# Optimization experiments

Measured on AMD Instinct MI355X. Metric: run time of the kernel, lower is better.

## Reference

```python
import jax, jax.numpy as jnp
import numpy as np

N_NODES = 100000
N_EDGES = 1600000
D = 64
N_LAYERS = 3
N_GRAPHS = 128
BN_EPS = 1e-5


def setup_inputs() -> dict:
    key = jax.random.key(0)
    k_x, k_e, k_b, k_w = jax.random.split(key, 4)
    x = jax.random.normal(k_x, (N_NODES, D), dtype=jnp.float32)
    edge_index = jax.random.randint(k_e, (2, N_EDGES), 0, N_NODES, dtype=jnp.int64)
    batch = jnp.sort(jax.random.randint(k_b, (N_NODES,), 0, N_GRAPHS, dtype=jnp.int64))
    Ws = jax.random.normal(k_w, (N_LAYERS, D, D), dtype=jnp.float32) * (1.0 / np.sqrt(D))
    bs = jnp.zeros((N_LAYERS, D), dtype=jnp.float32)
    gammas = jnp.ones((N_LAYERS, D), dtype=jnp.float32)
    betas = jnp.zeros((N_LAYERS, D), dtype=jnp.float32)
    return {"x": x, "edge_index": edge_index, "batch": batch,
            "Ws": Ws, "bs": bs, "gammas": gammas, "betas": betas}


def reference(x, edge_index, batch, Ws, bs, gammas, betas):
    N = x.shape[0]
    # GCN: add self-loops, symmetric normalization deg^{-1/2}_src * deg^{-1/2}_dst
    loop = jnp.arange(N, dtype=edge_index.dtype)
    src = jnp.concatenate([edge_index[0], loop])  # [E+N]
    dst = jnp.concatenate([edge_index[1], loop])
    deg = jax.ops.segment_sum(jnp.ones_like(dst, dtype=x.dtype), dst, num_segments=N)
    dinv = jnp.where(deg > 0, jax.lax.rsqrt(deg), 0.0)
    norm = dinv[src] * dinv[dst]  # [E+N]

    h = x
    for l in range(N_LAYERS):
        t = h @ Ws[l]                                    # [N,D] dense transform
        msg = t[src] * norm[:, None]                     # gather + scale [E+N,D]
        t = jax.ops.segment_sum(msg, dst, num_segments=N) + bs[l]
        # BatchNorm1d (training-style batch statistics, biased variance)
        mean = jnp.mean(t, axis=0)
        var = jnp.mean((t - mean) ** 2, axis=0)
        t = (t - mean) * jax.lax.rsqrt(var + BN_EPS) * gammas[l] + betas[l]
        h = jax.nn.relu(t)

    # global mean pool over graphs
    sums = jax.ops.segment_sum(h, batch, num_segments=N_GRAPHS)        # [G,D]
    counts = jax.ops.segment_sum(jnp.ones((N,), dtype=h.dtype), batch, num_segments=N_GRAPHS)
    return sums / jnp.maximum(counts, 1.0)[:, None]
```

## Files before the change

### kernel.cpp

```cpp
#include <hip/hip_runtime.h>
#include <hip/hip_bf16.h>

typedef __hip_bfloat16 bf16;
typedef short bf16x8 __attribute__((ext_vector_type(8)));
typedef float f32x4 __attribute__((ext_vector_type(4)));

#define NN 100000
#define NE 1600000
#define DD 64
#define NL 3
#define NG 128
#define BN_EPS 1e-5f
#define SCAN_BLK 98
#define TILE_ROWS 64
#define LSW 72
#define NT ((NN + TILE_ROWS - 1) / TILE_ROWS)
#define GB_NODES 48
#define GB_BLOCKS ((NN + GB_NODES - 1) / GB_NODES)
#define ECAP 1664
#define CSW_CAP (NE + 7 * NN)

#define NBUK 391
#define BUK_CAP 4608
#define OVF_CAP 8192
#define EPB 4096
#define NBB ((NE + EPB - 1) / EPB)

__device__ __forceinline__ int ld_src(const int* ei, int e, int is32) {
    return is32 ? ei[e] : ei[2 * e];
}
__device__ __forceinline__ int ld_dst(const int* ei, int e, int is32) {
    return is32 ? ei[NE + e] : ei[2 * NE + 2 * e];
}
__device__ __forceinline__ int ld_batch(const int* b, int n, int is32) {
    return is32 ? b[n] : b[2 * n];
}
__device__ __forceinline__ float bf2f(unsigned short u) {
    return __uint_as_float(((unsigned int)u) << 16);
}
__device__ __forceinline__ unsigned short f2bf(float x) {
    bf16 b = __float2bfloat16(x);
    return *reinterpret_cast<unsigned short*>(&b);
}
__device__ __forceinline__ void split_bf16(float x, unsigned short& hi, unsigned short& lo) {
    hi = f2bf(x);
    lo = f2bf(x - bf2f(hi));
}
__device__ __forceinline__ int pad8(int d) { return (d + 7) & ~7; }

__global__ __launch_bounds__(256) void bin_kernel(const int* __restrict__ ei,
                                                  int* __restrict__ deg_cnt,
                                                  int* __restrict__ bukcnt,
                                                  int* __restrict__ staging,
                                                  int* __restrict__ ovf_cnt,
                                                  int2* __restrict__ ovf) {
    __shared__ int hist[NBUK];
    __shared__ int base[NBUK];
    __shared__ int s_e;
    if (threadIdx.x == 0) s_e = 0;
    for (int i = threadIdx.x; i < NBUK; i += 256) hist[i] = 0;
    __syncthreads();
    if (ei[2 * threadIdx.x + 1] != 0) atomicOr(&s_e, 1);
    __syncthreads();
    int is32 = s_e;

    int e0 = blockIdx.x * EPB;
    int myb[16], mypack[16], myidx[16];
#pragma unroll
    for (int k = 0; k < 16; ++k) {
        int e = e0 + k * 256 + threadIdx.x;
        myb[k] = -1;
        if (e < NE) {
            int s = ld_src(ei, e, is32), d = ld_dst(ei, e, is32);
            int b = d >> 8;
            myb[k] = b;
            mypack[k] = (s << 8) | (d & 255);
            myidx[k] = atomicAdd(&hist[b], 1);
        }
    }
    __syncthreads();
    for (int i = threadIdx.x; i < NBUK; i += 256)
        if (hist[i]) base[i] = atomicAdd(&bukcnt[i], hist[i]);
    __syncthreads();
#pragma unroll
    for (int k = 0; k < 16; ++k) {
        if (myb[k] >= 0) {
            int slot = base[myb[k]] + myidx[k];
            if (slot < BUK_CAP) {
                staging[myb[k] * BUK_CAP + slot] = mypack[k];
            } else {
                int d = (myb[k] << 8) | (mypack[k] & 255);
                atomicAdd(&deg_cnt[d], 1);
                int o = atomicAdd(ovf_cnt, 1);
                if (o < OVF_CAP) ovf[o] = make_int2(mypack[k] >> 8, d);
            }
        }
    }
}

__global__ __launch_bounds__(256) void scan_part_kernel(int* __restrict__ deg_cnt,
                                                        const int* __restrict__ bukcnt,
                                                        const int* __restrict__ staging,
                                                        int* __restrict__ blocksum,
                                                        float* __restrict__ dinv) {
    __shared__ int hist[1024];
    __shared__ int s[256];
    for (int i = threadIdx.x; i < 1024; i += 256) hist[i] = 0;
    __syncthreads();
    int b4 = blockIdx.x * 4;
#pragma unroll
    for (int j = 0; j < 4; ++j) {
        int bk = b4 + j;
        if (bk < NBUK) {
            int n = min(bukcnt[bk], BUK_CAP);
            const int* st = staging + bk * BUK_CAP;
            for (int i = threadIdx.x; i < n; i += 256)
                atomicAdd(&hist[(j << 8) | (st[i] & 255)], 1);
        }
    }
    __syncthreads();
    int base = blockIdx.x * 1024 + threadIdx.x * 4;
    int t = 0;
    if (base < NN) {
        int4 ov = *(const int4*)(deg_cnt + base);
        int4 hv = *(const int4*)(hist + threadIdx.x * 4);
        int4 v = make_int4(ov.x + hv.x, ov.y + hv.y, ov.z + hv.z, ov.w + hv.w);
        *(int4*)(deg_cnt + base) = v;
        t = pad8(v.x) + pad8(v.y) + pad8(v.z) + pad8(v.w);
        float4 dv = make_float4(rsqrtf((float)v.x + 1.f), rsqrtf((float)v.y + 1.f),
                                rsqrtf((float)v.z + 1.f), rsqrtf((float)v.w + 1.f));
        *(float4*)(dinv + base) = dv;
    }
    s[threadIdx.x] = t;
    __syncthreads();
    for (int off = 128; off > 0; off >>= 1) {
        if (threadIdx.x < off) s[threadIdx.x] += s[threadIdx.x + off];
        __syncthreads();
    }
    if (threadIdx.x == 0) blocksum[blockIdx.x] = s[0];
}

__global__ __launch_bounds__(256) void scan_write_kernel(int* __restrict__ deg_cnt,
                                                         const int* __restrict__ blocksum,
                                                         int* __restrict__ rowptr) {
    __shared__ int sb[128];
    __shared__ int s[256];
    if (threadIdx.x < 128)
        sb[threadIdx.x] = (threadIdx.x < SCAN_BLK) ? blocksum[threadIdx.x] : 0;
    __syncthreads();
    for (int off = 1; off < 128; off <<= 1) {
        int a = 0;
        if (threadIdx.x < 128 && threadIdx.x >= off) a = sb[threadIdx.x - off];
        __syncthreads();
        if (threadIdx.x < 128) sb[threadIdx.x] += a;
        __syncthreads();
    }
    int blockpre = (blockIdx.x == 0) ? 0 : sb[blockIdx.x - 1];
    if (blockIdx.x == SCAN_BLK - 1 && threadIdx.x == 0)
        rowptr[NN] = sb[SCAN_BLK - 1];

    int base = blockIdx.x * 1024 + threadIdx.x * 4;
    int4 v = make_int4(0, 0, 0, 0);
    if (base < NN) v = *(const int4*)(deg_cnt + base);
    int p0 = pad8(v.x), p1 = pad8(v.y), p2 = pad8(v.z), p3 = pad8(v.w);
    int t = p0 + p1 + p2 + p3;
    s[threadIdx.x] = t;
    for (int off = 1; off < 256; off <<= 1) {
        __syncthreads();
        int a = (threadIdx.x >= off) ? s[threadIdx.x - off] : 0;
        __syncthreads();
        s[threadIdx.x] += a;
    }
    __syncthreads();
    int pre = blockpre + s[threadIdx.x] - t;
    if (base < NN) {
        rowptr[base] = pre;
        rowptr[base + 1] = pre + p0;
        rowptr[base + 2] = pre + p0 + p1;
        rowptr[base + 3] = pre + p0 + p1 + p2;
        *(int4*)(deg_cnt + base) = make_int4(0, 0, 0, 0);
    }
}

__global__ __launch_bounds__(256) void scatter_kernel(const int* __restrict__ bukcnt,
                                                      const int* __restrict__ staging,
                                                      const int* __restrict__ ovf_cnt,
                                                      const int2* __restrict__ ovf,
                                                      const int* __restrict__ rowptr,
                                                      int* __restrict__ cursor,
                                                      int* __restrict__ csw) {
    int b = blockIdx.x;
    if (b == NBUK) {
        int n = min(*ovf_cnt, OVF_CAP);
        for (int i = threadIdx.x; i < n; i += 256) {
            int2 e = ovf[i];
            int pos = rowptr[e.y] + atomicAdd(&cursor[e.y], 1);
            csw[pos] = (e.x + 1) << 7;
        }
        return;
    }
    int n = min(bukcnt[b], BUK_CAP);
    int nb = b << 8;
    const int* st = staging + b * BUK_CAP;
    for (int i = threadIdx.x; i < n; i += 256) {
        int v = st[i];
        int d = nb + (v & 255);
        int pos = rowptr[d] + atomicAdd(&cursor[d], 1);
        csw[pos] = ((v >> 8) + 1) << 7;
    }
}

__global__ __launch_bounds__(256) void gemm_kernel(const float* __restrict__ h,
                                                   const float* __restrict__ W,
                                                   const float* __restrict__ dinv,
                                                   const float* __restrict__ accum_prev,
                                                   const float* __restrict__ gamma,
                                                   const float* __restrict__ beta,
                                                   int use_bn, float alpha,
                                                   bf16* __restrict__ t,
                                                   float* __restrict__ accum_l) {
    if (blockIdx.x == 0 && threadIdx.x < 128) accum_l[threadIdx.x] = 0.f;

    __shared__ unsigned short ls_hi[TILE_ROWS * LSW];
    __shared__ unsigned short ls_lo[TILE_ROWS * LSW];
    __shared__ float ssc[DD], ssh[DD], sdinv[TILE_ROWS];
    int tid = threadIdx.x;
    if (tid < 64) {
        if (use_bn) {
            float S = accum_prev[tid], Q = accum_prev[64 + tid];
            float mean = S / (float)NN;
            float var = fmaxf(Q / (float)NN - mean * mean, 0.f);
            float sc = gamma[tid] * rsqrtf(var + BN_EPS);
            ssc[tid] = sc;
            ssh[tid] = beta[tid] - mean * sc;
        } else {
            ssc[tid] = 1.f;
            ssh[tid] = 0.f;
        }
    }

    int lane = tid & 63;
    int wv = tid >> 6;
    int lr = lane & 15;
    int lg = lane >> 4;

    bf16x8 bhi[2][4], blo[2][4];
#pragma unroll
    for (int ks = 0; ks < 2; ++ks)
#pragma unroll
        for (int nt = 0; nt < 4; ++nt)
#pragma unroll
            for (int e = 0; e < 8; ++e) {
                float wval = W[(ks * 32 + lg * 8 + e) * DD + nt * 16 + lr];
                unsigned short hi, lo;
                split_bf16(wval, hi, lo);
                bhi[ks][nt][e] = (short)hi;
                blo[ks][nt][e] = (short)lo;
            }
    __syncthreads();

    for (int tile = blockIdx.x; tile < NT; tile += gridDim.x) {
        int row0 = tile * TILE_ROWS;
        int nrows = min(TILE_ROWS, NN - row0);
        if (tid < 64) sdinv[tid] = (row0 + tid < NN) ? dinv[row0 + tid] : 0.f;
#pragma unroll
        for (int it = 0; it < 4; ++it) {
            int flat = (tid + it * 256) * 4;
            int gflat = row0 * DD + flat;
            if (gflat < NN * DD) {
                float4 hv = *(const float4*)(h + gflat);
                int c0 = flat & 63;
                float4 s4 = *(const float4*)(ssc + c0);
                float4 b4 = *(const float4*)(ssh + c0);
                float x0 = hv.x * s4.x + b4.x;
                float x1 = hv.y * s4.y + b4.y;
                float x2 = hv.z * s4.z + b4.z;
                float x3 = hv.w * s4.w + b4.w;
                x0 = fmaxf(x0, x0 * alpha);
                x1 = fmaxf(x1, x1 * alpha);
                x2 = fmaxf(x2, x2 * alpha);
                x3 = fmaxf(x3, x3 * alpha);
                unsigned short h0, l0, h1, l1, h2, l2, h3, l3;
                split_bf16(x0, h0, l0);
                split_bf16(x1, h1, l1);
                split_bf16(x2, h2, l2);
                split_bf16(x3, h3, l3);
                int row = flat >> 6;
                *(ushort4*)(ls_hi + row * LSW + c0) = make_ushort4(h0, h1, h2, h3);
                *(ushort4*)(ls_lo + row * LSW + c0) = make_ushort4(l0, l1, l2, l3);
            }
        }
        __syncthreads();

        f32x4 acc[4];
#pragma unroll
        for (int nt = 0; nt < 4; ++nt) acc[nt] = (f32x4){0.f, 0.f, 0.f, 0.f};

#pragma unroll
        for (int ks = 0; ks < 2; ++ks) {
            int aoff = (wv * 16 + lr) * LSW + ks * 32 + lg * 8;
            bf16x8 a_hi = *(const bf16x8*)(ls_hi + aoff);
            bf16x8 a_lo = *(const bf16x8*)(ls_lo + aoff);
#pragma unroll
            for (int nt = 0; nt < 4; ++nt) {
                acc[nt] = __builtin_amdgcn_mfma_f32_16x16x32_bf16(a_hi, bhi[ks][nt],
                                                                  acc[nt], 0, 0, 0);
                acc[nt] = __builtin_amdgcn_mfma_f32_16x16x32_bf16(a_hi, blo[ks][nt],
                                                                  acc[nt], 0, 0, 0);
                acc[nt] = __builtin_amdgcn_mfma_f32_16x16x32_bf16(a_lo, bhi[ks][nt],
                                                                  acc[nt], 0, 0, 0);
            }
        }
        __syncthreads();

#pragma unroll
        for (int nt = 0; nt < 4; ++nt)
#pragma unroll
            for (int rg = 0; rg < 4; ++rg) {
                int orow = wv * 16 + lg * 4 + rg;
                ls_hi[orow * LSW + nt * 16 + lr] = f2bf(acc[nt][rg] * sdinv[orow]);
            }
        __syncthreads();
#pragma unroll
        for (int it = 0; it < 2; ++it) {
            int flat8 = (tid + it * 256) * 8;
            int row = flat8 >> 6, c = flat8 & 63;
            if (row < nrows) {
                uint4 v = *(const uint4*)(ls_hi + row * LSW + c);
                *(uint4*)((unsigned short*)t + (size_t)(row0 + row) * DD + c) = v;
            }
        }
        __syncthreads();
    }
}

__device__ __forceinline__ void batch8(const int* __restrict__ ep, int j,
                                       const char* __restrict__ tbase, int f2,
                                       float& acc) {
    int4 a0 = *(const int4*)(ep + j);
    int4 a1 = *(const int4*)(ep + j + 4);
    unsigned short r[8];
    r[0] = *(const unsigned short*)(tbase + (unsigned)(a0.x + f2));
    r[1] = *(const unsigned short*)(tbase + (unsigned)(a0.y + f2));
    r[2] = *(const unsigned short*)(tbase + (unsigned)(a0.z + f2));
    r[3] = *(const unsigned short*)(tbase + (unsigned)(a0.w + f2));
    r[4] = *(const unsigned short*)(tbase + (unsigned)(a1.x + f2));
    r[5] = *(const unsigned short*)(tbase + (unsigned)(a1.y + f2));
    r[6] = *(const unsigned short*)(tbase + (unsigned)(a1.z + f2));
    r[7] = *(const unsigned short*)(tbase + (unsigned)(a1.w + f2));
    float s01 = bf2f(r[0]) + bf2f(r[1]), s23 = bf2f(r[2]) + bf2f(r[3]);
    float s45 = bf2f(r[4]) + bf2f(r[5]), s67 = bf2f(r[6]) + bf2f(r[7]);
    acc += (s01 + s23) + (s45 + s67);
}

__device__ __forceinline__ void batch8x2(const int* __restrict__ ep, int jA, int jB,
                                         const char* __restrict__ tbase, int f2,
                                         float& accA, float& accB) {
    int4 aA0 = *(const int4*)(ep + jA), aA1 = *(const int4*)(ep + jA + 4);
    int4 aB0 = *(const int4*)(ep + jB), aB1 = *(const int4*)(ep + jB + 4);
    unsigned short rA[8], rB[8];
    rA[0] = *(const unsigned short*)(tbase + (unsigned)(aA0.x + f2));
    rA[1] = *(const unsigned short*)(tbase + (unsigned)(aA0.y + f2));
    rA[2] = *(const unsigned short*)(tbase + (unsigned)(aA0.z + f2));
    rA[3] = *(const unsigned short*)(tbase + (unsigned)(aA0.w + f2));
    rA[4] = *(const unsigned short*)(tbase + (unsigned)(aA1.x + f2));
    rA[5] = *(const unsigned short*)(tbase + (unsigned)(aA1.y + f2));
    rA[6] = *(const unsigned short*)(tbase + (unsigned)(aA1.z + f2));
    rA[7] = *(const unsigned short*)(tbase + (unsigned)(aA1.w + f2));
    rB[0] = *(const unsigned short*)(tbase + (unsigned)(aB0.x + f2));
    rB[1] = *(const unsigned short*)(tbase + (unsigned)(aB0.y + f2));
    rB[2] = *(const unsigned short*)(tbase + (unsigned)(aB0.z + f2));
    rB[3] = *(const unsigned short*)(tbase + (unsigned)(aB0.w + f2));
    rB[4] = *(const unsigned short*)(tbase + (unsigned)(aB1.x + f2));
    rB[5] = *(const unsigned short*)(tbase + (unsigned)(aB1.y + f2));
    rB[6] = *(const unsigned short*)(tbase + (unsigned)(aB1.z + f2));
    rB[7] = *(const unsigned short*)(tbase + (unsigned)(aB1.w + f2));
    float sA01 = bf2f(rA[0]) + bf2f(rA[1]), sA23 = bf2f(rA[2]) + bf2f(rA[3]);
    float sA45 = bf2f(rA[4]) + bf2f(rA[5]), sA67 = bf2f(rA[6]) + bf2f(rA[7]);
    accA += (sA01 + sA23) + (sA45 + sA67);
    float sB01 = bf2f(rB[0]) + bf2f(rB[1]), sB23 = bf2f(rB[2]) + bf2f(rB[3]);
    float sB45 = bf2f(rB[4]) + bf2f(rB[5]), sB67 = bf2f(rB[6]) + bf2f(rB[7]);
    accB += (sB01 + sB23) + (sB45 + sB67);
}

__device__ __forceinline__ void batch8x4(const int* __restrict__ ep, int jA, int jB,
                                         int jC, int jD,
                                         const char* __restrict__ tbase, int f2,
                                         float& accA, float& accB, float& accC,
                                         float& accD) {
    int4 aA0 = *(const int4*)(ep + jA), aA1 = *(const int4*)(ep + jA + 4);
    int4 aB0 = *(const int4*)(ep + jB), aB1 = *(const int4*)(ep + jB + 4);
    int4 aC0 = *(const int4*)(ep + jC), aC1 = *(const int4*)(ep + jC + 4);
    int4 aD0 = *(const int4*)(ep + jD), aD1 = *(const int4*)(ep + jD + 4);
    unsigned short rA[8], rB[8], rC[8], rD[8];
    rA[0] = *(const unsigned short*)(tbase + (unsigned)(aA0.x + f2));
    rA[1] = *(const unsigned short*)(tbase + (unsigned)(aA0.y + f2));
    rA[2] = *(const unsigned short*)(tbase + (unsigned)(aA0.z + f2));
    rA[3] = *(const unsigned short*)(tbase + (unsigned)(aA0.w + f2));
    rA[4] = *(const unsigned short*)(tbase + (unsigned)(aA1.x + f2));
    rA[5] = *(const unsigned short*)(tbase + (unsigned)(aA1.y + f2));
    rA[6] = *(const unsigned short*)(tbase + (unsigned)(aA1.z + f2));
    rA[7] = *(const unsigned short*)(tbase + (unsigned)(aA1.w + f2));
    rB[0] = *(const unsigned short*)(tbase + (unsigned)(aB0.x + f2));
    rB[1] = *(const unsigned short*)(tbase + (unsigned)(aB0.y + f2));
    rB[2] = *(const unsigned short*)(tbase + (unsigned)(aB0.z + f2));
    rB[3] = *(const unsigned short*)(tbase + (unsigned)(aB0.w + f2));
    rB[4] = *(const unsigned short*)(tbase + (unsigned)(aB1.x + f2));
    rB[5] = *(const unsigned short*)(tbase + (unsigned)(aB1.y + f2));
    rB[6] = *(const unsigned short*)(tbase + (unsigned)(aB1.z + f2));
    rB[7] = *(const unsigned short*)(tbase + (unsigned)(aB1.w + f2));
    rC[0] = *(const unsigned short*)(tbase + (unsigned)(aC0.x + f2));
    rC[1] = *(const unsigned short*)(tbase + (unsigned)(aC0.y + f2));
    rC[2] = *(const unsigned short*)(tbase + (unsigned)(aC0.z + f2));
    rC[3] = *(const unsigned short*)(tbase + (unsigned)(aC0.w + f2));
    rC[4] = *(const unsigned short*)(tbase + (unsigned)(aC1.x + f2));
    rC[5] = *(const unsigned short*)(tbase + (unsigned)(aC1.y + f2));
    rC[6] = *(const unsigned short*)(tbase + (unsigned)(aC1.z + f2));
    rC[7] = *(const unsigned short*)(tbase + (unsigned)(aC1.w + f2));
    rD[0] = *(const unsigned short*)(tbase + (unsigned)(aD0.x + f2));
    rD[1] = *(const unsigned short*)(tbase + (unsigned)(aD0.y + f2));
    rD[2] = *(const unsigned short*)(tbase + (unsigned)(aD0.z + f2));
    rD[3] = *(const unsigned short*)(tbase + (unsigned)(aD0.w + f2));
    rD[4] = *(const unsigned short*)(tbase + (unsigned)(aD1.x + f2));
    rD[5] = *(const unsigned short*)(tbase + (unsigned)(aD1.y + f2));
    rD[6] = *(const unsigned short*)(tbase + (unsigned)(aD1.z + f2));
    rD[7] = *(const unsigned short*)(tbase + (unsigned)(aD1.w + f2));
    float sA01 = bf2f(rA[0]) + bf2f(rA[1]), sA23 = bf2f(rA[2]) + bf2f(rA[3]);
    float sA45 = bf2f(rA[4]) + bf2f(rA[5]), sA67 = bf2f(rA[6]) + bf2f(rA[7]);
    accA += (sA01 + sA23) + (sA45 + sA67);
    float sB01 = bf2f(rB[0]) + bf2f(rB[1]), sB23 = bf2f(rB[2]) + bf2f(rB[3]);
    float sB45 = bf2f(rB[4]) + bf2f(rB[5]), sB67 = bf2f(rB[6]) + bf2f(rB[7]);
    accB += (sB01 + sB23) + (sB45 + sB67);
    float sC01 = bf2f(rC[0]) + bf2f(rC[1]), sC23 = bf2f(rC[2]) + bf2f(rC[3]);
    float sC45 = bf2f(rC[4]) + bf2f(rC[5]), sC67 = bf2f(rC[6]) + bf2f(rC[7]);
    accC += (sC01 + sC23) + (sC45 + sC67);
    float sD01 = bf2f(rD[0]) + bf2f(rD[1]), sD23 = bf2f(rD[2]) + bf2f(rD[3]);
    float sD45 = bf2f(rD[4]) + bf2f(rD[5]), sD67 = bf2f(rD[6]) + bf2f(rD[7]);
    accD += (sD01 + sD23) + (sD45 + sD67);
}

__device__ __forceinline__ void run_quad(const int* __restrict__ ep,
                                         const char* __restrict__ tbase, int f2,
                                         int jA, int eA, int jB, int eB,
                                         int jC, int eC, int jD, int eD,
                                         float& accA, float& accB, float& accC,
                                         float& accD) {
    while (jA < eA && jB < eB && jC < eC && jD < eD) {
        batch8x4(ep, jA, jB, jC, jD, tbase, f2, accA, accB, accC, accD);
        jA += 8; jB += 8; jC += 8; jD += 8;
    }
    while (jA < eA && jB < eB) { batch8x2(ep, jA, jB, tbase, f2, accA, accB); jA += 8; jB += 8; }
    while (jC < eC && jD < eD) { batch8x2(ep, jC, jD, tbase, f2, accC, accD); jC += 8; jD += 8; }
    while (jA < eA && jC < eC) { batch8x2(ep, jA, jC, tbase, f2, accA, accC); jA += 8; jC += 8; }
    while (jA < eA && jD < eD) { batch8x2(ep, jA, jD, tbase, f2, accA, accD); jA += 8; jD += 8; }
    while (jB < eB && jC < eC) { batch8x2(ep, jB, jC, tbase, f2, accB, accC); jB += 8; jC += 8; }
    while (jB < eB && jD < eD) { batch8x2(ep, jB, jD, tbase, f2, accB, accD); jB += 8; jD += 8; }
    while (jA < eA) { batch8(ep, jA, tbase, f2, accA); jA += 8; }
    while (jB < eB) { batch8(ep, jB, tbase, f2, accB); jB += 8; }
    while (jC < eC) { batch8(ep, jC, tbase, f2, accC); jC += 8; }
    while (jD < eD) { batch8(ep, jD, tbase, f2, accD); jD += 8; }
}

__global__ __launch_bounds__(256) void gather_kernel(const bf16* __restrict__ t,
                                                     const float* __restrict__ dinv,
                                                     const float* __restrict__ bias,
                                                     const int* __restrict__ rowptr,
                                                     const int* __restrict__ csw,
                                                     float* __restrict__ h,
                                                     float* __restrict__ accum_l) {
    __shared__ __attribute__((aligned(16))) int se[ECAP];
    __shared__ int srp[GB_NODES + 1];
    __shared__ float s_sum[256], s_sq[256];

    int f = threadIdx.x & 63;
    int wv = threadIdx.x >> 6;
    int nb0 = blockIdx.x * GB_NODES;
    int nloc = min(GB_NODES, NN - nb0);

    for (int i = threadIdx.x; i <= nloc; i += 256) srp[i] = rowptr[nb0 + i];
    __syncthreads();
    int ebase = srp[0];
    int nE = srp[nloc] - ebase;
    bool staged = (nE <= ECAP);
    if (staged) {
        for (int i = threadIdx.x * 4; i < nE; i += 1024)
            *(int4*)(se + i) = *(const int4*)(csw + ebase + i);
    }
    __syncthreads();

    const char* tbase = (const char*)t - 128;
    int f2 = f * 2;
    const unsigned short* tf = (const unsigned short*)t + f;
    float bb = bias[f];
    float sum = 0.f, sq = 0.f;

    for (int q = wv; 4 * q < nloc; q += 4) {
        int d0 = 4 * q;
        int nA = nb0 + d0, nB = nA + 1, nC = nA + 2, nD = nA + 3;
        float accA = bf2f(tf[(size_t)nA * DD]);
        float accB = bf2f(tf[(size_t)nB * DD]);
        float accC = bf2f(tf[(size_t)nC * DD]);
        float accD = bf2f(tf[(size_t)nD * DD]);
        int jA = srp[d0] - ebase, eA = srp[d0 + 1] - ebase;
        int jB = eA, eB = srp[d0 + 2] - ebase;
        int jC = eB, eC = srp[d0 + 3] - ebase;
        int jD = eC, eD = srp[d0 + 4] - ebase;

        if (staged)
            run_quad(se, tbase, f2, jA, eA, jB, eB, jC, eC, jD, eD, accA, accB, accC, accD);
        else
            run_quad(csw + ebase, tbase, f2, jA, eA, jB, eB, jC, eC, jD, eD,
                     accA, accB, accC, accD);

        float diA = dinv[nA], diB = dinv[nB], diC = dinv[nC], diD = dinv[nD];
        accA = accA * diA + bb;
        accB = accB * diB + bb;
        accC = accC * diC + bb;
        accD = accD * diD + bb;
        h[(size_t)nA * DD + f] = accA;
        h[(size_t)nB * DD + f] = accB;
        h[(size_t)nC * DD + f] = accC;
        h[(size_t)nD * DD + f] = accD;
        sum += accA + accB + accC + accD;
        sq += accA * accA + accB * accB + accC * accC + accD * accD;
    }
    s_sum[threadIdx.x] = sum;
    s_sq[threadIdx.x] = sq;
    __syncthreads();
    if (threadIdx.x < 64) {
        sum = s_sum[f] + s_sum[64 + f] + s_sum[128 + f] + s_sum[192 + f];
        sq = s_sq[f] + s_sq[64 + f] + s_sq[128 + f] + s_sq[192 + f];
        atomicAdd(&accum_l[f], sum);
        atomicAdd(&accum_l[64 + f], sq);
    }
}

#define POOL_CHUNK 128
__global__ __launch_bounds__(256) void pool_kernel(const float* __restrict__ hraw,
                                                   const float* __restrict__ accum_l,
                                                   const float* __restrict__ gamma,
                                                   const float* __restrict__ beta,
                                                   const int* __restrict__ batch,
                                                   float* __restrict__ pool,
                                                   float* __restrict__ counts) {
    __shared__ float ssc[64], ssh[64];
    __shared__ int s_b;
    if (threadIdx.x == 0) s_b = 0;
    if (threadIdx.x < 64) {
        float S = accum_l[threadIdx.x], Q = accum_l[64 + threadIdx.x];
        float mean = S / (float)NN;
        float var = fmaxf(Q / (float)NN - mean * mean, 0.f);
        float sc = gamma[threadIdx.x] * rsqrtf(var + BN_EPS);
        ssc[threadIdx.x] = sc;
        ssh[threadIdx.x] = beta[threadIdx.x] - mean * sc;
    }
    __syncthreads();
    if (batch[NN - 1024 + 2 * threadIdx.x + 1] != 0) atomicOr(&s_b, 1);
    __syncthreads();
    int is32 = s_b;
    int f = threadIdx.x & 63, rg = threadIdx.x >> 6;
    float sc = ssc[f], sh = ssh[f];
    int base = blockIdx.x * POOL_CHUNK;
    float acc = 0.f, cnt = 0.f;
    int cur = -1;
    for (int i = rg; i < POOL_CHUNK; i += 4) {
        int n = base + i;
        if (n >= NN) break;
        int g = ld_batch(batch, n, is32);
        if (g != cur) {
            if (cur >= 0) {
                atomicAdd(&pool[cur * DD + f], acc);
                if (f == 0) atomicAdd(&counts[cur], cnt);
            }
            acc = 0.f;
            cnt = 0.f;
            cur = g;
        }
        acc += fmaxf(hraw[(size_t)n * DD + f] * sc + sh, 0.f);
        cnt += 1.f;
    }
    if (cur >= 0) {
        atomicAdd(&pool[cur * DD + f], acc);
        if (f == 0) atomicAdd(&counts[cur], cnt);
    }
}

__global__ __launch_bounds__(256) void final_kernel(const float* __restrict__ pool,
                                                    const float* __restrict__ counts,
                                                    float* __restrict__ out) {
    int i = blockIdx.x * 256 + threadIdx.x;
    if (i < NG * DD) {
        int g = i >> 6;
        out[i] = pool[i] / fmaxf(counts[g], 1.0f);
    }
}

extern "C" void kernel_launch(void* const* d_in, const int* in_sizes, int n_in,
                              void* d_out, int out_size, void* d_ws, size_t ws_size,
                              hipStream_t stream) {
    const float* x = (const float*)d_in[0];
    const int* edge_index = (const int*)d_in[1];
    const int* batch = (const int*)d_in[2];
    const float* Ws = (const float*)d_in[3];
    const float* bs = (const float*)d_in[4];
    const float* gammas = (const float*)d_in[5];
    const float* betas = (const float*)d_in[6];
    float* out = (float*)d_out;

    float* h = (float*)d_ws;
    bf16* zrow = (bf16*)(h + (size_t)NN * DD);
    bf16* t = zrow + DD;
    int* csw = (int*)(t + (size_t)NN * DD);
    float* dinv = (float*)(csw + CSW_CAP);
    int* deg_cnt = (int*)(dinv + NN);
    float* pool = (float*)(deg_cnt + NN);
    float* counts = pool + NG * DD;
    int* bukcnt = (int*)(counts + NG);
    int* ovf_cnt = bukcnt + NBUK;
    int* rowptr = ovf_cnt + 1;
    float* accum = (float*)(rowptr + NN + 1);
    int* blocksum = (int*)(accum + NL * 128);
    int2* ovf = (int2*)(blocksum + 128);
    int* staging = (int*)h;

    hipMemsetAsync(deg_cnt, 0, (NN + NG * DD + NG + NBUK + 1) * sizeof(int), stream);
    hipMemsetAsync(csw, 0, (size_t)CSW_CAP * sizeof(int), stream);
    hipMemsetAsync(zrow, 0, DD * sizeof(bf16), stream);

    bin_kernel<<<NBB, 256, 0, stream>>>(edge_index, deg_cnt, bukcnt, staging,
                                        ovf_cnt, ovf);
    scan_part_kernel<<<SCAN_BLK, 256, 0, stream>>>(deg_cnt, bukcnt, staging, blocksum,
                                                   dinv);
    scan_write_kernel<<<SCAN_BLK, 256, 0, stream>>>(deg_cnt, blocksum, rowptr);
    scatter_kernel<<<NBUK + 1, 256, 0, stream>>>(bukcnt, staging, ovf_cnt, ovf, rowptr,
                                                 deg_cnt, csw);

    for (int l = 0; l < NL; ++l) {
        const float* hin = (l == 0) ? x : h;
        float alpha = (l == 0) ? 1.0f : 0.0f;
        gemm_kernel<<<NT, 256, 0, stream>>>(hin, Ws + (size_t)l * DD * DD, dinv,
                                            accum + (l - 1 >= 0 ? l - 1 : 0) * 128,
                                            gammas + (l - 1 >= 0 ? l - 1 : 0) * DD,
                                            betas + (l - 1 >= 0 ? l - 1 : 0) * DD,
                                            (l > 0) ? 1 : 0, alpha, t, accum + l * 128);
        gather_kernel<<<GB_BLOCKS, 256, 0, stream>>>(t, dinv, bs + l * DD, rowptr, csw, h,
                                                     accum + l * 128);
    }

    pool_kernel<<<(NN + POOL_CHUNK - 1) / POOL_CHUNK, 256, 0, stream>>>(
        h, accum + 2 * 128, gammas + 2 * DD, betas + 2 * DD, batch, pool, counts);
    final_kernel<<<(NG * DD + 255) / 256, 256, 0, stream>>>(pool, counts, out);
}
```

Baseline: 494.6 us.

## Fuse scatter with layer-0 GEMM, precompute weight fragments, fold final into pool

```diff
diff --git a/kernel.cpp b/kernel.cpp
--- a/kernel.cpp
+++ b/kernel.cpp
@@ -1,5 +1,6 @@
 #include <hip/hip_runtime.h>
 #include <hip/hip_bf16.h>
+#include <stdint.h>
 
 typedef __hip_bfloat16 bf16;
 typedef short bf16x8 __attribute__((ext_vector_type(8)));
@@ -19,6 +20,7 @@
 #define GB_BLOCKS ((NN + GB_NODES - 1) / GB_NODES)
 #define ECAP 1664
 #define CSW_CAP (NE + 7 * NN)
+#define WFL 8192
 
 #define NBUK 391
 #define BUK_CAP 4608
@@ -142,7 +144,27 @@
 
 __global__ __launch_bounds__(256) void scan_write_kernel(int* __restrict__ deg_cnt,
                                                          const int* __restrict__ blocksum,
-                                                         int* __restrict__ rowptr) {
+                                                         int* __restrict__ rowptr,
+                                                         const float* __restrict__ Ws,
+                                                         unsigned short* __restrict__ wfrag) {
+    if (blockIdx.x >= SCAN_BLK) {
+        int l = blockIdx.x - SCAN_BLK;
+        const float* W = Ws + (size_t)l * DD * DD;
+        unsigned short* wf = wfrag + (size_t)l * WFL;
+        for (int slot = threadIdx.x; slot < 512; slot += 256) {
+            int lane = slot & 63, nt = (slot >> 6) & 3, ks = slot >> 8;
+            int lr = lane & 15, lg = lane >> 4;
+#pragma unroll
+            for (int e = 0; e < 8; ++e) {
+                float wval = W[(ks * 32 + lg * 8 + e) * DD + nt * 16 + lr];
+                unsigned short hi, lo;
+                split_bf16(wval, hi, lo);
+                wf[((0 * 2 + ks) * 4 + nt) * 512 + lane * 8 + e] = hi;
+                wf[((1 * 2 + ks) * 4 + nt) * 512 + lane * 8 + e] = lo;
+            }
+        }
+        return;
+    }
     __shared__ int sb[128];
     __shared__ int s[256];
     if (threadIdx.x < 128)
@@ -182,14 +204,13 @@
     }
 }
 
-__global__ __launch_bounds__(256) void scatter_kernel(const int* __restrict__ bukcnt,
-                                                      const int* __restrict__ staging,
-                                                      const int* __restrict__ ovf_cnt,
-                                                      const int2* __restrict__ ovf,
-                                                      const int* __restrict__ rowptr,
-                                                      int* __restrict__ cursor,
-                                                      int* __restrict__ csw) {
-    int b = blockIdx.x;
+__device__ __forceinline__ void scatter_body(int b, const int* __restrict__ bukcnt,
+                                             const int* __restrict__ staging,
+                                             const int* __restrict__ ovf_cnt,
+                                             const int2* __restrict__ ovf,
+                                             const int* __restrict__ rowptr,
+                                             int* __restrict__ cursor,
+                                             int* __restrict__ csw) {
     if (b == NBUK) {
         int n = min(*ovf_cnt, OVF_CAP);
         for (int i = threadIdx.x; i < n; i += 256) {
@@ -210,20 +231,24 @@
     }
 }
 
-__global__ __launch_bounds__(256) void gemm_kernel(const float* __restrict__ h,
-                                                   const float* __restrict__ W,
-                                                   const float* __restrict__ dinv,
-                                                   const float* __restrict__ accum_prev,
-                                                   const float* __restrict__ gamma,
-                                                   const float* __restrict__ beta,
-                                                   int use_bn, float alpha,
-                                                   bf16* __restrict__ t,
-                                                   float* __restrict__ accum_l) {
-    if (blockIdx.x == 0 && threadIdx.x < 128) accum_l[threadIdx.x] = 0.f;
-
-    __shared__ unsigned short ls_hi[TILE_ROWS * LSW];
-    __shared__ unsigned short ls_lo[TILE_ROWS * LSW];
-    __shared__ float ssc[DD], ssh[DD], sdinv[TILE_ROWS];
+struct GemmSmem {
+    unsigned short ls_hi[TILE_ROWS * LSW];
+    unsigned short ls_lo[TILE_ROWS * LSW];
+    float ssc[DD], ssh[DD], sdinv[TILE_ROWS];
+};
+
+__device__ __forceinline__ void gemm_body(GemmSmem& sm,
+                                          const float* __restrict__ h,
+                                          const unsigned short* __restrict__ wf,
+                                          const float* __restrict__ dinv,
+                                          const float* __restrict__ accum_prev,
+                                          const float* __restrict__ gamma,
+                                          const float* __restrict__ beta,
+                                          int use_bn, float alpha,
+                                          bf16* __restrict__ t,
+                                          float* __restrict__ accum_l,
+                                          int do_zero, int tile0, int tstride) {
+    if (do_zero && threadIdx.x < 128) accum_l[threadIdx.x] = 0.f;
     int tid = threadIdx.x;
     if (tid < 64) {
         if (use_bn) {
@@ -231,11 +256,11 @@
             float mean = S / (float)NN;
             float var = fmaxf(Q / (float)NN - mean * mean, 0.f);
             float sc = gamma[tid] * rsqrtf(var + BN_EPS);
-            ssc[tid] = sc;
-            ssh[tid] = beta[tid] - mean * sc;
+            sm.ssc[tid] = sc;
+            sm.ssh[tid] = beta[tid] - mean * sc;
         } else {
-            ssc[tid] = 1.f;
-            ssh[tid] = 0.f;
+            sm.ssc[tid] = 1.f;
+            sm.ssh[tid] = 0.f;
         }
     }
 
@@ -248,21 +273,16 @@
 #pragma unroll
     for (int ks = 0; ks < 2; ++ks)
 #pragma unroll
-        for (int nt = 0; nt < 4; ++nt)
-#pragma unroll
-            for (int e = 0; e < 8; ++e) {
-                float wval = W[(ks * 32 + lg * 8 + e) * DD + nt * 16 + lr];
-                unsigned short hi, lo;
-                split_bf16(wval, hi, lo);
-                bhi[ks][nt][e] = (short)hi;
-                blo[ks][nt][e] = (short)lo;
-            }
-    __syncthreads();
-
-    for (int tile = blockIdx.x; tile < NT; tile += gridDim.x) {
+        for (int nt = 0; nt < 4; ++nt) {
+            bhi[ks][nt] = *(const bf16x8*)(wf + ((0 * 2 + ks) * 4 + nt) * 512 + lane * 8);
+            blo[ks][nt] = *(const bf16x8*)(wf + ((1 * 2 + ks) * 4 + nt) * 512 + lane * 8);
+        }
+    __syncthreads();
+
+    for (int tile = tile0; tile < NT; tile += tstride) {
         int row0 = tile * TILE_ROWS;
         int nrows = min(TILE_ROWS, NN - row0);
-        if (tid < 64) sdinv[tid] = (row0 + tid < NN) ? dinv[row0 + tid] : 0.f;
+        if (tid < 64) sm.sdinv[tid] = (row0 + tid < NN) ? dinv[row0 + tid] : 0.f;
 #pragma unroll
         for (int it = 0; it < 4; ++it) {
             int flat = (tid + it * 256) * 4;
@@ -270,8 +290,8 @@
             if (gflat < NN * DD) {
                 float4 hv = *(const float4*)(h + gflat);
                 int c0 = flat & 63;
-                float4 s4 = *(const float4*)(ssc + c0);
-                float4 b4 = *(const float4*)(ssh + c0);
+                float4 s4 = *(const float4*)(sm.ssc + c0);
+                float4 b4 = *(const float4*)(sm.ssh + c0);
                 float x0 = hv.x * s4.x + b4.x;
                 float x1 = hv.y * s4.y + b4.y;
                 float x2 = hv.z * s4.z + b4.z;
@@ -286,8 +306,8 @@
                 split_bf16(x2, h2, l2);
                 split_bf16(x3, h3, l3);
                 int row = flat >> 6;
-                *(ushort4*)(ls_hi + row * LSW + c0) = make_ushort4(h0, h1, h2, h3);
-                *(ushort4*)(ls_lo + row * LSW + c0) = make_ushort4(l0, l1, l2, l3);
+                *(ushort4*)(sm.ls_hi + row * LSW + c0) = make_ushort4(h0, h1, h2, h3);
+                *(ushort4*)(sm.ls_lo + row * LSW + c0) = make_ushort4(l0, l1, l2, l3);
             }
         }
         __syncthreads();
@@ -299,8 +319,8 @@
 #pragma unroll
         for (int ks = 0; ks < 2; ++ks) {
             int aoff = (wv * 16 + lr) * LSW + ks * 32 + lg * 8;
-            bf16x8 a_hi = *(const bf16x8*)(ls_hi + aoff);
-            bf16x8 a_lo = *(const bf16x8*)(ls_lo + aoff);
+            bf16x8 a_hi = *(const bf16x8*)(sm.ls_hi + aoff);
+            bf16x8 a_lo = *(const bf16x8*)(sm.ls_lo + aoff);
 #pragma unroll
             for (int nt = 0; nt < 4; ++nt) {
                 acc[nt] = __builtin_amdgcn_mfma_f32_16x16x32_bf16(a_hi, bhi[ks][nt],
@@ -318,7 +338,7 @@
 #pragma unroll
             for (int rg = 0; rg < 4; ++rg) {
                 int orow = wv * 16 + lg * 4 + rg;
-                ls_hi[orow * LSW + nt * 16 + lr] = f2bf(acc[nt][rg] * sdinv[orow]);
+                sm.ls_hi[orow * LSW + nt * 16 + lr] = f2bf(acc[nt][rg] * sm.sdinv[orow]);
             }
         __syncthreads();
 #pragma unroll
@@ -326,12 +346,42 @@
             int flat8 = (tid + it * 256) * 8;
             int row = flat8 >> 6, c = flat8 & 63;
             if (row < nrows) {
-                uint4 v = *(const uint4*)(ls_hi + row * LSW + c);
+                uint4 v = *(const uint4*)(sm.ls_hi + row * LSW + c);
                 *(uint4*)((unsigned short*)t + (size_t)(row0 + row) * DD + c) = v;
             }
         }
         __syncthreads();
     }
+}
+
+__global__ __launch_bounds__(256) void scatter_gemm_kernel(
+    const int* __restrict__ bukcnt, const int* __restrict__ staging,
+    const int* __restrict__ ovf_cnt, const int2* __restrict__ ovf,
+    const int* __restrict__ rowptr, int* __restrict__ cursor, int* __restrict__ csw,
+    const float* __restrict__ x, const unsigned short* __restrict__ wfrag,
+    const float* __restrict__ dinv, bf16* __restrict__ t, float* __restrict__ accum_l) {
+    __shared__ GemmSmem sm;
+    int b = blockIdx.x;
+    if (b <= NBUK) {
+        scatter_body(b, bukcnt, staging, ovf_cnt, ovf, rowptr, cursor, csw);
+        return;
+    }
+    int g = b - (NBUK + 1);
+    gemm_body(sm, x, wfrag, dinv, nullptr, nullptr, nullptr, 0, 1.0f, t, accum_l,
+              g == 0, g, gridDim.x - (NBUK + 1));
+}
+
+__global__ __launch_bounds__(256) void gemm_kernel(const float* __restrict__ h,
+                                                   const unsigned short* __restrict__ wfrag,
+                                                   const float* __restrict__ dinv,
+                                                   const float* __restrict__ accum_prev,
+                                                   const float* __restrict__ gamma,
+                                                   const float* __restrict__ beta,
+                                                   bf16* __restrict__ t,
+                                                   float* __restrict__ accum_l) {
+    __shared__ GemmSmem sm;
+    gemm_body(sm, h, wfrag, dinv, accum_prev, gamma, beta, 1, 0.0f, t, accum_l,
+              blockIdx.x == 0, blockIdx.x, gridDim.x);
 }
 
 __device__ __forceinline__ void batch8(const int* __restrict__ ep, int j,
@@ -542,9 +592,13 @@
                                                    const float* __restrict__ beta,
                                                    const int* __restrict__ batch,
                                                    float* __restrict__ pool,
-                                                   float* __restrict__ counts) {
+                                                   float* __restrict__ counts,
+                                                   int* __restrict__ done,
+                                                   float* __restrict__ out) {
     __shared__ float ssc[64], ssh[64];
+    __shared__ float scnt[NG];
     __shared__ int s_b;
+    __shared__ int isLast;
     if (threadIdx.x == 0) s_b = 0;
     if (threadIdx.x < 64) {
         float S = accum_l[threadIdx.x], Q = accum_l[64 + threadIdx.x];
@@ -583,15 +637,16 @@
         atomicAdd(&pool[cur * DD + f], acc);
         if (f == 0) atomicAdd(&counts[cur], cnt);
     }
-}
-
-__global__ __launch_bounds__(256) void final_kernel(const float* __restrict__ pool,
-                                                    const float* __restrict__ counts,
-                                                    float* __restrict__ out) {
-    int i = blockIdx.x * 256 + threadIdx.x;
-    if (i < NG * DD) {
-        int g = i >> 6;
-        out[i] = pool[i] / fmaxf(counts[g], 1.0f);
+    __threadfence();
+    if (threadIdx.x == 0) isLast = (atomicAdd(done, 1) == (int)gridDim.x - 1);
+    __syncthreads();
+    if (isLast) {
+        for (int i = threadIdx.x; i < NG; i += 256) scnt[i] = atomicAdd(&counts[i], 0.f);
+        __syncthreads();
+        for (int i = threadIdx.x; i < NG * DD; i += 256) {
+            float v = atomicAdd(&pool[i], 0.f);
+            out[i] = v / fmaxf(scnt[i >> 6], 1.0f);
+        }
     }
 }
 
@@ -617,13 +672,16 @@
     float* counts = pool + NG * DD;
     int* bukcnt = (int*)(counts + NG);
     int* ovf_cnt = bukcnt + NBUK;
-    int* rowptr = ovf_cnt + 1;
+    int* done = ovf_cnt + 1;
+    int* rowptr = done + 1;
     float* accum = (float*)(rowptr + NN + 1);
     int* blocksum = (int*)(accum + NL * 128);
-    int2* ovf = (int2*)(blocksum + 128);
+    unsigned short* wfrag =
+        (unsigned short*)(((uintptr_t)(blocksum + 128) + 15) & ~(uintptr_t)15);
+    int2* ovf = (int2*)(wfrag + (size_t)NL * WFL);
     int* staging = (int*)h;
 
-    hipMemsetAsync(deg_cnt, 0, (NN + NG * DD + NG + NBUK + 1) * sizeof(int), stream);
+    hipMemsetAsync(deg_cnt, 0, (NN + NG * DD + NG + NBUK + 2) * sizeof(int), stream);
     hipMemsetAsync(csw, 0, (size_t)CSW_CAP * sizeof(int), stream);
     hipMemsetAsync(zrow, 0, DD * sizeof(bf16), stream);
 
@@ -631,23 +689,25 @@
                                         ovf_cnt, ovf);
     scan_part_kernel<<<SCAN_BLK, 256, 0, stream>>>(deg_cnt, bukcnt, staging, blocksum,
                                                    dinv);
-    scan_write_kernel<<<SCAN_BLK, 256, 0, stream>>>(deg_cnt, blocksum, rowptr);
-    scatter_kernel<<<NBUK + 1, 256, 0, stream>>>(bukcnt, staging, ovf_cnt, ovf, rowptr,
-                                                 deg_cnt, csw);
-
-    for (int l = 0; l < NL; ++l) {
-        const float* hin = (l == 0) ? x : h;
-        float alpha = (l == 0) ? 1.0f : 0.0f;
-        gemm_kernel<<<NT, 256, 0, stream>>>(hin, Ws + (size_t)l * DD * DD, dinv,
-                                            accum + (l - 1 >= 0 ? l - 1 : 0) * 128,
-                                            gammas + (l - 1 >= 0 ? l - 1 : 0) * DD,
-                                            betas + (l - 1 >= 0 ? l - 1 : 0) * DD,
-                                            (l > 0) ? 1 : 0, alpha, t, accum + l * 128);
+    scan_write_kernel<<<SCAN_BLK + NL, 256, 0, stream>>>(deg_cnt, blocksum, rowptr,
+                                                         Ws, wfrag);
+    scatter_gemm_kernel<<<NBUK + 1 + NT, 256, 0, stream>>>(
+        bukcnt, staging, ovf_cnt, ovf, rowptr, deg_cnt, csw,
+        x, wfrag, dinv, t, accum + 0 * 128);
+    gather_kernel<<<GB_BLOCKS, 256, 0, stream>>>(t, dinv, bs + 0 * DD, rowptr, csw, h,
+                                                 accum + 0 * 128);
+
+    for (int l = 1; l < NL; ++l) {
+        gemm_kernel<<<NT, 256, 0, stream>>>(h, wfrag + (size_t)l * WFL, dinv,
+                                            accum + (l - 1) * 128,
+                                            gammas + (size_t)(l - 1) * DD,
+                                            betas + (size_t)(l - 1) * DD,
+                                            t, accum + l * 128);
         gather_kernel<<<GB_BLOCKS, 256, 0, stream>>>(t, dinv, bs + l * DD, rowptr, csw, h,
                                                      accum + l * 128);
     }
 
     pool_kernel<<<(NN + POOL_CHUNK - 1) / POOL_CHUNK, 256, 0, stream>>>(
-        h, accum + 2 * 128, gammas + 2 * DD, betas + 2 * DD, batch, pool, counts);
-    final_kernel<<<(NG * DD + 255) / 256, 256, 0, stream>>>(pool, counts, out);
-}
+        h, accum + 2 * 128, gammas + 2 * DD, betas + 2 * DD, batch, pool, counts,
+        done, out);
+}
```

New measurement: 536.3 us. 1.08x slower.
